# Performance work log

Hardware: AMD Instinct MI355X
Metric: run time of the kernel (lower is better)

## Reference

```python
import jax, jax.numpy as jnp
import numpy as np

HIDDEN = 1024
INTER = 2048
NUM_EXPERTS = 8
TOPK = 2
STD = 0.02


def setup_inputs() -> dict:
    key = jax.random.key(0)
    k1, k2, k3, k4 = jax.random.split(key, 4)
    return {
        "hidden_states": jax.random.normal(k1, (1, 2048, HIDDEN), dtype=jnp.float32),
        "w1": jax.random.normal(k2, (NUM_EXPERTS, 2 * INTER, HIDDEN), dtype=jnp.float32) * STD,
        "w2": jax.random.normal(k3, (NUM_EXPERTS, HIDDEN, INTER), dtype=jnp.float32) * STD,
        "router_w": jax.random.normal(k4, (NUM_EXPERTS, HIDDEN), dtype=jnp.float32) * STD,
    }


def reference(hidden_states, w1, w2, router_w):
    # renormalize=False (the torch forward's default)
    orig_shape = hidden_states.shape
    dtype = hidden_states.dtype
    x = hidden_states.reshape(-1, orig_shape[-1])          # [T, H]
    E = w1.shape[0]

    gating = x @ router_w.T                                 # [T, E]
    probs = jax.nn.softmax(gating.astype(jnp.float32), axis=-1)
    topk_w, sel = jax.lax.top_k(probs, TOPK)                # [T, K]
    topk_w = topk_w.astype(dtype)

    # Per-(token, expert) combine weight; equivalent to the dispatch/sort/
    # grouped-GEMM/index_add path since unselected experts get weight 0.
    combine = (jax.nn.one_hot(sel, E, dtype=dtype) * topk_w[..., None]).sum(axis=1)  # [T, E]

    h = jnp.einsum('td,eid->tei', x, w1)                    # [T, E, 2*INTER]
    gate = jax.nn.silu(h[..., :INTER])
    y = h[..., INTER:] * gate                               # [T, E, INTER]
    out = jnp.einsum('tei,ehi,te->th', y, w2, combine)      # [T, H]
    return out.reshape(orig_shape)
```

## Files before the change

kernel.cpp:

```cpp
#include <hip/hip_runtime.h>
#include <hip/hip_bf16.h>
#include <math.h>

#define T_TOKENS 2048
#define HID 1024
#define INTER 2048
#define NE 8

typedef __attribute__((ext_vector_type(8))) __bf16 bf16x8;
typedef __attribute__((ext_vector_type(4))) __bf16 bf16x4;
typedef __attribute__((ext_vector_type(4))) float f32x4;

#define WS_COUNTS   0u
#define WS_OFFSETS  64u
#define WS_SEL      128u
#define WS_SELW     16512u
#define WS_ROWTOK   32896u
#define WS_ROWW     49280u
#define WS_XB       131072u
#define WS_Y        (131072u + 4194304u)

__device__ __forceinline__ void gload_lds16(const void* g, void* l) {
    __builtin_amdgcn_global_load_lds(
        (const __attribute__((address_space(1))) unsigned int*)g,
        (__attribute__((address_space(3))) unsigned int*)l, 16, 0, 0);
}

__device__ __forceinline__ bf16x8 cvt8(float4 a, float4 b) {
    bf16x8 r;
    r[0] = (__bf16)a.x; r[1] = (__bf16)a.y; r[2] = (__bf16)a.z; r[3] = (__bf16)a.w;
    r[4] = (__bf16)b.x; r[5] = (__bf16)b.y; r[6] = (__bf16)b.z; r[7] = (__bf16)b.w;
    return r;
}

__device__ __forceinline__ bf16x8 ldsfrag(const __bf16* base, int row, int g) {
    return *(const bf16x8*)((const char*)base + row * 64 +
                            ((g ^ ((row >> 1) & 3)) << 4));
}

__global__ __launch_bounds__(256) void moe_router(
    const float* __restrict__ x, const float* __restrict__ rw,
    int* __restrict__ counts, int* __restrict__ sel, float* __restrict__ selw,
    __bf16* __restrict__ xb)
{
    int wave = threadIdx.x >> 6;
    int lane = threadIdx.x & 63;
    int t = blockIdx.x * 4 + wave;
    if (t >= T_TOKENS) return;

    const float4* x4  = (const float4*)x + (size_t)t * (HID / 4);
    const float4* rw4 = (const float4*)rw;

    float acc[NE];
#pragma unroll
    for (int e = 0; e < NE; ++e) acc[e] = 0.f;
#pragma unroll
    for (int q = 0; q < 4; ++q) {
        int idx = q * 64 + lane;
        float4 xv = x4[idx];
        bf16x4 c;
        c[0] = (__bf16)xv.x; c[1] = (__bf16)xv.y; c[2] = (__bf16)xv.z; c[3] = (__bf16)xv.w;
        *(bf16x4*)(xb + (size_t)t * HID + idx * 4) = c;
#pragma unroll
        for (int e = 0; e < NE; ++e) {
            float4 rv = rw4[e * (HID / 4) + idx];
            acc[e] += xv.x * rv.x + xv.y * rv.y + xv.z * rv.z + xv.w * rv.w;
        }
    }
#pragma unroll
    for (int off = 32; off; off >>= 1)
#pragma unroll
        for (int e = 0; e < NE; ++e) acc[e] += __shfl_xor(acc[e], off, 64);

    if (lane == 0) {
        float m = acc[0];
#pragma unroll
        for (int e = 1; e < NE; ++e) m = fmaxf(m, acc[e]);
        float p[NE], s = 0.f;
#pragma unroll
        for (int e = 0; e < NE; ++e) { p[e] = expf(acc[e] - m); s += p[e]; }
        float inv = 1.f / s;
        int i0 = 0;
#pragma unroll
        for (int e = 1; e < NE; ++e) if (p[e] > p[i0]) i0 = e;
        int i1 = (i0 == 0) ? 1 : 0;
#pragma unroll
        for (int e = 0; e < NE; ++e) if (e != i0 && p[e] > p[i1]) i1 = e;
        sel[t * 2 + 0] = i0; selw[t * 2 + 0] = p[i0] * inv;
        sel[t * 2 + 1] = i1; selw[t * 2 + 1] = p[i1] * inv;
        atomicAdd(&counts[i0], 1);
        atomicAdd(&counts[i1], 1);
    }
}

__global__ __launch_bounds__(256) void moe_scan_assign(
    const int* __restrict__ counts, int* __restrict__ offsets,
    const int* __restrict__ sel, const float* __restrict__ selw,
    int* __restrict__ row_token, float* __restrict__ row_w)
{
    __shared__ int soff[NE];
    __shared__ int scur[NE];
    if (threadIdx.x == 0) {
        int off = 0;
        for (int e = 0; e < NE; ++e) { soff[e] = off; off += counts[e]; }
    }
    if (threadIdx.x < NE) scur[threadIdx.x] = 0;
    __syncthreads();
    if (threadIdx.x < NE) offsets[threadIdx.x] = soff[threadIdx.x];
    for (int t = threadIdx.x; t < T_TOKENS; t += 256) {
#pragma unroll
        for (int k = 0; k < 2; ++k) {
            int e = sel[t * 2 + k];
            int slot = atomicAdd(&scur[e], 1);
            int r = soff[e] + slot;
            row_token[r] = t;
            row_w[r] = selw[t * 2 + k];
        }
    }
}

__global__ __launch_bounds__(256, 4) void moe_gemm1(
    const __bf16* __restrict__ xb, const float* __restrict__ w1,
    const int* __restrict__ row_token, const int* __restrict__ counts,
    const int* __restrict__ offsets, __bf16* __restrict__ y)
{
    int e = blockIdx.z;
    int cnt = counts[e];
    int row0 = blockIdx.y * 128;
    if (row0 >= cnt) return;
    int col0 = blockIdx.x * 64;
    int base = offsets[e];

    __shared__ __bf16 As[2][128 * 32];
    __shared__ __bf16 Bg[2][64 * 32];
    __shared__ __bf16 Bu[2][64 * 32];

    int tid = threadIdx.x;
    int lane = tid & 63;
    int wid = tid >> 6;
    int gq = tid & 3;
    int sw = (tid >> 3) & 3;

    const __bf16* srcA[2];
    int dstA[2];
#pragma unroll
    for (int i = 0; i < 2; ++i) {
        int r = i * 64 + (tid >> 2);
        int rl = row0 + r; if (rl > cnt - 1) rl = cnt - 1;
        int tok = row_token[base + rl];
        srcA[i] = xb + (size_t)tok * HID + ((gq ^ sw) << 3);
        dstA[i] = i * 4096 + tid * 16;
    }
    int rb = tid >> 2;
    const float* srcBg = w1 + ((size_t)e * 2 * INTER + col0 + rb) * HID + (gq << 3);
    const float* srcBu = srcBg + (size_t)INTER * HID;
    int offB = rb * 64 + ((gq ^ sw) << 4);

#pragma unroll
    for (int i = 0; i < 2; ++i) gload_lds16(srcA[i], (char*)As[0] + dstA[i]);
    {
        float4 g0 = *(const float4*)(srcBg);
        float4 g1 = *(const float4*)(srcBg + 4);
        float4 u0 = *(const float4*)(srcBu);
        float4 u1 = *(const float4*)(srcBu + 4);
        *(bf16x8*)((char*)Bg[0] + offB) = cvt8(g0, g1);
        *(bf16x8*)((char*)Bu[0] + offB) = cvt8(u0, u1);
    }
    __syncthreads();

    int wr = (wid >> 1) * 64, wc = (wid & 1) * 32;
    f32x4 ag[4][2] = {}, au[4][2] = {};

    for (int t = 0; t < 32; ++t) {
        int cur = t & 1;
        float4 g0, g1, u0, u1;
        bool pre = (t < 31);
        if (pre) {
            int k0 = (t + 1) * 32;
#pragma unroll
            for (int i = 0; i < 2; ++i)
                gload_lds16(srcA[i] + k0, (char*)As[cur ^ 1] + dstA[i]);
            g0 = *(const float4*)(srcBg + k0);
            g1 = *(const float4*)(srcBg + k0 + 4);
            u0 = *(const float4*)(srcBu + k0);
            u1 = *(const float4*)(srcBu + k0 + 4);
        }
        const __bf16* Ab = As[cur];
        const __bf16* Bgb = Bg[cur];
        const __bf16* Bub = Bu[cur];
        {
            int kg = lane >> 4;
            bf16x8 a[4], bg[2], bu[2];
#pragma unroll
            for (int m = 0; m < 4; ++m) a[m] = ldsfrag(Ab, wr + m * 16 + (lane & 15), kg);
#pragma unroll
            for (int n = 0; n < 2; ++n) {
                bg[n] = ldsfrag(Bgb, wc + n * 16 + (lane & 15), kg);
                bu[n] = ldsfrag(Bub, wc + n * 16 + (lane & 15), kg);
            }
#pragma unroll
            for (int m = 0; m < 4; ++m)
#pragma unroll
                for (int n = 0; n < 2; ++n) {
                    ag[m][n] = __builtin_amdgcn_mfma_f32_16x16x32_bf16(a[m], bg[n], ag[m][n], 0, 0, 0);
                    au[m][n] = __builtin_amdgcn_mfma_f32_16x16x32_bf16(a[m], bu[n], au[m][n], 0, 0, 0);
                }
        }
        if (pre) {
            *(bf16x8*)((char*)Bg[cur ^ 1] + offB) = cvt8(g0, g1);
            *(bf16x8*)((char*)Bu[cur ^ 1] + offB) = cvt8(u0, u1);
        }
        __syncthreads();
    }

#pragma unroll
    for (int m = 0; m < 4; ++m) {
#pragma unroll
        for (int j = 0; j < 4; ++j) {
            int rl = wr + m * 16 + ((lane >> 4) << 2) + j;
            if (row0 + rl >= cnt) continue;
            size_t yrow = (size_t)(base + row0 + rl) * INTER;
#pragma unroll
            for (int n = 0; n < 2; ++n) {
                float g = ag[m][n][j], u = au[m][n][j];
                float s = g / (1.f + __expf(-g));
                y[yrow + col0 + wc + n * 16 + (lane & 15)] = (__bf16)(s * u);
            }
        }
    }
}

__global__ __launch_bounds__(256, 4) void moe_gemm2(
    const __bf16* __restrict__ y, const float* __restrict__ w2,
    const float* __restrict__ row_w, const int* __restrict__ row_token,
    const int* __restrict__ counts, const int* __restrict__ offsets,
    float* __restrict__ out)
{
    int e = blockIdx.z;
    int cnt = counts[e];
    int row0 = (blockIdx.y >> 1) * 128;
    if (row0 >= cnt) return;
    int kbase = (blockIdx.y & 1) * (INTER / 2);
    int col0 = blockIdx.x * 64;
    int base = offsets[e];

    __shared__ __bf16 As[2][128 * 32];
    __shared__ __bf16 Bs[2][64 * 32];

    int tid = threadIdx.x;
    int lane = tid & 63;
    int wid = tid >> 6;
    int gq = tid & 3;
    int sw = (tid >> 3) & 3;

    const __bf16* srcA[2];
    int dstA[2];
#pragma unroll
    for (int i = 0; i < 2; ++i) {
        int r = i * 64 + (tid >> 2);
        int rl = row0 + r; if (rl > cnt - 1) rl = cnt - 1;
        srcA[i] = y + (size_t)(base + rl) * INTER + kbase + ((gq ^ sw) << 3);
        dstA[i] = i * 4096 + tid * 16;
    }
    int rb = tid >> 2;
    const float* srcB = w2 + ((size_t)e * HID + col0 + rb) * INTER + kbase + (gq << 3);
    int offB = rb * 64 + ((gq ^ sw) << 4);

#pragma unroll
    for (int i = 0; i < 2; ++i) gload_lds16(srcA[i], (char*)As[0] + dstA[i]);
    {
        float4 b0 = *(const float4*)(srcB);
        float4 b1 = *(const float4*)(srcB + 4);
        *(bf16x8*)((char*)Bs[0] + offB) = cvt8(b0, b1);
    }
    __syncthreads();

    int wr = (wid >> 1) * 64, wc = (wid & 1) * 32;
    f32x4 acc[4][2] = {};

    for (int t = 0; t < 32; ++t) {
        int cur = t & 1;
        float4 b0, b1;
        bool pre = (t < 31);
        if (pre) {
            int k0 = (t + 1) * 32;
#pragma unroll
            for (int i = 0; i < 2; ++i)
                gload_lds16(srcA[i] + k0, (char*)As[cur ^ 1] + dstA[i]);
            b0 = *(const float4*)(srcB + k0);
            b1 = *(const float4*)(srcB + k0 + 4);
        }
        const __bf16* Ab = As[cur];
        const __bf16* Bb = Bs[cur];
        {
            int kg = lane >> 4;
            bf16x8 a[4], b[2];
#pragma unroll
            for (int m = 0; m < 4; ++m) a[m] = ldsfrag(Ab, wr + m * 16 + (lane & 15), kg);
#pragma unroll
            for (int n = 0; n < 2; ++n) b[n] = ldsfrag(Bb, wc + n * 16 + (lane & 15), kg);
#pragma unroll
            for (int m = 0; m < 4; ++m)
#pragma unroll
                for (int n = 0; n < 2; ++n)
                    acc[m][n] = __builtin_amdgcn_mfma_f32_16x16x32_bf16(a[m], b[n], acc[m][n], 0, 0, 0);
        }
        if (pre) {
            *(bf16x8*)((char*)Bs[cur ^ 1] + offB) = cvt8(b0, b1);
        }
        __syncthreads();
    }

#pragma unroll
    for (int m = 0; m < 4; ++m) {
#pragma unroll
        for (int j = 0; j < 4; ++j) {
            int rl = wr + m * 16 + ((lane >> 4) << 2) + j;
            if (row0 + rl >= cnt) continue;
            float wgt = row_w[base + row0 + rl];
            int tok = row_token[base + row0 + rl];
#pragma unroll
            for (int n = 0; n < 2; ++n)
                atomicAdd(&out[(size_t)tok * HID + col0 + wc + n * 16 + (lane & 15)],
                          acc[m][n][j] * wgt);
        }
    }
}

extern "C" void kernel_launch(void* const* d_in, const int* in_sizes, int n_in,
                              void* d_out, int out_size, void* d_ws, size_t ws_size,
                              hipStream_t stream) {
    const float* x  = (const float*)d_in[0];
    const float* w1 = (const float*)d_in[1];
    const float* w2 = (const float*)d_in[2];
    const float* rw = (const float*)d_in[3];
    float* out = (float*)d_out;

    char* ws = (char*)d_ws;
    int*    counts     = (int*)(ws + WS_COUNTS);
    int*    offsets    = (int*)(ws + WS_OFFSETS);
    int*    sel        = (int*)(ws + WS_SEL);
    float*  selw       = (float*)(ws + WS_SELW);
    int*    row_token  = (int*)(ws + WS_ROWTOK);
    float*  row_w      = (float*)(ws + WS_ROWW);
    __bf16* xb         = (__bf16*)(ws + WS_XB);
    __bf16* y          = (__bf16*)(ws + WS_Y);

    hipMemsetAsync(ws, 0, 128, stream);
    hipMemsetAsync(out, 0, (size_t)T_TOKENS * HID * sizeof(float), stream);

    moe_router<<<T_TOKENS / 4, 256, 0, stream>>>(x, rw, counts, sel, selw, xb);
    moe_scan_assign<<<1, 256, 0, stream>>>(counts, offsets, sel, selw,
                                           row_token, row_w);
    moe_gemm1<<<dim3(INTER / 64, 16, NE), 256, 0, stream>>>(
        xb, w1, row_token, counts, offsets, y);
    moe_gemm2<<<dim3(HID / 64, 32, NE), 256, 0, stream>>>(
        y, w2, row_w, row_token, counts, offsets, out);
}
```

Before: 423.8 us.

## Load fp32 weights directly to LDS and convert at fragment read time

Both grouped GEMMs now stream the fp32 weight tiles straight into shared memory with global_load_lds instead of loading through registers and converting before the LDS store. The bf16 conversion moves into the fragment read, and the K step grows to 64 with an XOR swizzle on both tiles. Double buffering is dropped for a single buffer bracketed by two barriers, and occupancy hints fall from 4 to 3 blocks. GEMM2 switches to a 128-wide N tile with a 4-way K split. The goal is to cut register pressure and the VALU conversion cost, at the price of more LDS (fp32 B tiles) and no overlap between loads and MFMA work.

```diff
diff --git a/kernel.cpp b/kernel.cpp
--- a/kernel.cpp
+++ b/kernel.cpp
@@ -33,9 +33,16 @@
     return r;
 }
 
-__device__ __forceinline__ bf16x8 ldsfrag(const __bf16* base, int row, int g) {
-    return *(const bf16x8*)((const char*)base + row * 64 +
-                            ((g ^ ((row >> 1) & 3)) << 4));
+__device__ __forceinline__ bf16x8 ldsfragA(const __bf16* base, int row, int g) {
+    return *(const bf16x8*)((const char*)base + row * 128 + ((g ^ (row & 7)) << 4));
+}
+
+__device__ __forceinline__ bf16x8 ldsfragB(const float* base, int row, int kc4) {
+    const char* p = (const char*)base + row * 256;
+    int s = row & 7;
+    float4 p0 = *(const float4*)(p + ((((kc4 << 1)    ) ^ s) << 4));
+    float4 p1 = *(const float4*)(p + ((((kc4 << 1) | 1) ^ s) << 4));
+    return cvt8(p0, p1);
 }
 
 __global__ __launch_bounds__(256) void moe_router(
@@ -119,7 +126,7 @@
     }
 }
 
-__global__ __launch_bounds__(256, 4) void moe_gemm1(
+__global__ __launch_bounds__(256, 3) void moe_gemm1(
     const __bf16* __restrict__ xb, const float* __restrict__ w1,
     const int* __restrict__ row_token, const int* __restrict__ counts,
     const int* __restrict__ offsets, __bf16* __restrict__ y)
@@ -131,72 +138,60 @@
     int col0 = blockIdx.x * 64;
     int base = offsets[e];
 
-    __shared__ __bf16 As[2][128 * 32];
-    __shared__ __bf16 Bg[2][64 * 32];
-    __shared__ __bf16 Bu[2][64 * 32];
+    __shared__ __bf16 As[128 * 64];
+    __shared__ float  Bs[128 * 64];
 
     int tid = threadIdx.x;
     int lane = tid & 63;
     int wid = tid >> 6;
-    int gq = tid & 3;
-    int sw = (tid >> 3) & 3;
-
-    const __bf16* srcA[2];
-    int dstA[2];
-#pragma unroll
-    for (int i = 0; i < 2; ++i) {
-        int r = i * 64 + (tid >> 2);
+
+    const __bf16* srcA[4];
+    int dstA[4];
+#pragma unroll
+    for (int i = 0; i < 4; ++i) {
+        int ii = wid * 4 + i;
+        int r = ii * 8 + (lane >> 3);
         int rl = row0 + r; if (rl > cnt - 1) rl = cnt - 1;
         int tok = row_token[base + rl];
-        srcA[i] = xb + (size_t)tok * HID + ((gq ^ sw) << 3);
-        dstA[i] = i * 4096 + tid * 16;
-    }
-    int rb = tid >> 2;
-    const float* srcBg = w1 + ((size_t)e * 2 * INTER + col0 + rb) * HID + (gq << 3);
-    const float* srcBu = srcBg + (size_t)INTER * HID;
-    int offB = rb * 64 + ((gq ^ sw) << 4);
-
-#pragma unroll
-    for (int i = 0; i < 2; ++i) gload_lds16(srcA[i], (char*)As[0] + dstA[i]);
+        srcA[i] = xb + (size_t)tok * HID + (((lane & 7) ^ (r & 7)) << 3);
+        dstA[i] = ii * 1024 + lane * 16;
+    }
+    const float* srcB[2];
+    int dstB0 = wid * 8192 + lane * 16;
     {
-        float4 g0 = *(const float4*)(srcBg);
-        float4 g1 = *(const float4*)(srcBg + 4);
-        float4 u0 = *(const float4*)(srcBu);
-        float4 u1 = *(const float4*)(srcBu + 4);
-        *(bf16x8*)((char*)Bg[0] + offB) = cvt8(g0, g1);
-        *(bf16x8*)((char*)Bu[0] + offB) = cvt8(u0, u1);
-    }
-    __syncthreads();
+        int rev = wid * 32 + (lane >> 4);
+        int rod = rev + 4;
+        int grow_ev = (rev < 64) ? (col0 + rev) : (INTER + col0 + rev - 64);
+        int grow_od = (rod < 64) ? (col0 + rod) : (INTER + col0 + rod - 64);
+        srcB[0] = w1 + ((size_t)e * 2 * INTER + grow_ev) * HID
+                     + (((lane & 15) ^ (rev & 7)) << 2);
+        srcB[1] = w1 + ((size_t)e * 2 * INTER + grow_od) * HID
+                     + (((lane & 15) ^ (rod & 7)) << 2);
+    }
 
     int wr = (wid >> 1) * 64, wc = (wid & 1) * 32;
     f32x4 ag[4][2] = {}, au[4][2] = {};
 
-    for (int t = 0; t < 32; ++t) {
-        int cur = t & 1;
-        float4 g0, g1, u0, u1;
-        bool pre = (t < 31);
-        if (pre) {
-            int k0 = (t + 1) * 32;
-#pragma unroll
-            for (int i = 0; i < 2; ++i)
-                gload_lds16(srcA[i] + k0, (char*)As[cur ^ 1] + dstA[i]);
-            g0 = *(const float4*)(srcBg + k0);
-            g1 = *(const float4*)(srcBg + k0 + 4);
-            u0 = *(const float4*)(srcBu + k0);
-            u1 = *(const float4*)(srcBu + k0 + 4);
-        }
-        const __bf16* Ab = As[cur];
-        const __bf16* Bgb = Bg[cur];
-        const __bf16* Bub = Bu[cur];
-        {
-            int kg = lane >> 4;
+    for (int k0 = 0; k0 < HID; k0 += 64) {
+        __syncthreads();
+#pragma unroll
+        for (int i = 0; i < 4; ++i)
+            gload_lds16(srcA[i] + k0, (char*)As + dstA[i]);
+#pragma unroll
+        for (int i = 0; i < 8; ++i)
+            gload_lds16(srcB[i & 1] + (i >> 1) * (8 * HID) + k0,
+                        (char*)Bs + dstB0 + i * 1024);
+        __syncthreads();
+#pragma unroll
+        for (int ks = 0; ks < 2; ++ks) {
+            int kc4 = ks * 4 + (lane >> 4);
             bf16x8 a[4], bg[2], bu[2];
 #pragma unroll
-            for (int m = 0; m < 4; ++m) a[m] = ldsfrag(Ab, wr + m * 16 + (lane & 15), kg);
+            for (int m = 0; m < 4; ++m) a[m] = ldsfragA(As, wr + m * 16 + (lane & 15), kc4);
 #pragma unroll
             for (int n = 0; n < 2; ++n) {
-                bg[n] = ldsfrag(Bgb, wc + n * 16 + (lane & 15), kg);
-                bu[n] = ldsfrag(Bub, wc + n * 16 + (lane & 15), kg);
+                bg[n] = ldsfragB(Bs, wc + n * 16 + (lane & 15), kc4);
+                bu[n] = ldsfragB(Bs, 64 + wc + n * 16 + (lane & 15), kc4);
             }
 #pragma unroll
             for (int m = 0; m < 4; ++m)
@@ -206,11 +201,6 @@
                     au[m][n] = __builtin_amdgcn_mfma_f32_16x16x32_bf16(a[m], bu[n], au[m][n], 0, 0, 0);
                 }
         }
-        if (pre) {
-            *(bf16x8*)((char*)Bg[cur ^ 1] + offB) = cvt8(g0, g1);
-            *(bf16x8*)((char*)Bu[cur ^ 1] + offB) = cvt8(u0, u1);
-        }
-        __syncthreads();
     }
 
 #pragma unroll
@@ -230,7 +220,7 @@
     }
 }
 
-__global__ __launch_bounds__(256, 4) void moe_gemm2(
+__global__ __launch_bounds__(256, 3) void moe_gemm2(
     const __bf16* __restrict__ y, const float* __restrict__ w2,
     const float* __restrict__ row_w, const int* __restrict__ row_token,
     const int* __restrict__ counts, const int* __restrict__ offsets,
@@ -238,77 +228,67 @@
 {
     int e = blockIdx.z;
     int cnt = counts[e];
-    int row0 = (blockIdx.y >> 1) * 128;
+    int row0 = (blockIdx.y >> 2) * 128;
     if (row0 >= cnt) return;
-    int kbase = (blockIdx.y & 1) * (INTER / 2);
-    int col0 = blockIdx.x * 64;
+    int kbase = (blockIdx.y & 3) * (INTER / 4);
+    int col0 = blockIdx.x * 128;
     int base = offsets[e];
 
-    __shared__ __bf16 As[2][128 * 32];
-    __shared__ __bf16 Bs[2][64 * 32];
+    __shared__ __bf16 As[128 * 64];
+    __shared__ float  Bs[128 * 64];
 
     int tid = threadIdx.x;
     int lane = tid & 63;
     int wid = tid >> 6;
-    int gq = tid & 3;
-    int sw = (tid >> 3) & 3;
-
-    const __bf16* srcA[2];
-    int dstA[2];
-#pragma unroll
-    for (int i = 0; i < 2; ++i) {
-        int r = i * 64 + (tid >> 2);
+
+    const __bf16* srcA[4];
+    int dstA[4];
+#pragma unroll
+    for (int i = 0; i < 4; ++i) {
+        int ii = wid * 4 + i;
+        int r = ii * 8 + (lane >> 3);
         int rl = row0 + r; if (rl > cnt - 1) rl = cnt - 1;
-        srcA[i] = y + (size_t)(base + rl) * INTER + kbase + ((gq ^ sw) << 3);
-        dstA[i] = i * 4096 + tid * 16;
-    }
-    int rb = tid >> 2;
-    const float* srcB = w2 + ((size_t)e * HID + col0 + rb) * INTER + kbase + (gq << 3);
-    int offB = rb * 64 + ((gq ^ sw) << 4);
-
-#pragma unroll
-    for (int i = 0; i < 2; ++i) gload_lds16(srcA[i], (char*)As[0] + dstA[i]);
+        srcA[i] = y + (size_t)(base + rl) * INTER + kbase + (((lane & 7) ^ (r & 7)) << 3);
+        dstA[i] = ii * 1024 + lane * 16;
+    }
+    const float* srcB[2];
+    int dstB0 = wid * 8192 + lane * 16;
     {
-        float4 b0 = *(const float4*)(srcB);
-        float4 b1 = *(const float4*)(srcB + 4);
-        *(bf16x8*)((char*)Bs[0] + offB) = cvt8(b0, b1);
-    }
-    __syncthreads();
-
-    int wr = (wid >> 1) * 64, wc = (wid & 1) * 32;
-    f32x4 acc[4][2] = {};
-
-    for (int t = 0; t < 32; ++t) {
-        int cur = t & 1;
-        float4 b0, b1;
-        bool pre = (t < 31);
-        if (pre) {
-            int k0 = (t + 1) * 32;
-#pragma unroll
-            for (int i = 0; i < 2; ++i)
-                gload_lds16(srcA[i] + k0, (char*)As[cur ^ 1] + dstA[i]);
-            b0 = *(const float4*)(srcB + k0);
-            b1 = *(const float4*)(srcB + k0 + 4);
-        }
-        const __bf16* Ab = As[cur];
-        const __bf16* Bb = Bs[cur];
-        {
-            int kg = lane >> 4;
-            bf16x8 a[4], b[2];
-#pragma unroll
-            for (int m = 0; m < 4; ++m) a[m] = ldsfrag(Ab, wr + m * 16 + (lane & 15), kg);
-#pragma unroll
-            for (int n = 0; n < 2; ++n) b[n] = ldsfrag(Bb, wc + n * 16 + (lane & 15), kg);
+        int rev = wid * 32 + (lane >> 4);
+        int rod = rev + 4;
+        srcB[0] = w2 + ((size_t)e * HID + col0 + rev) * INTER + kbase
+                     + (((lane & 15) ^ (rev & 7)) << 2);
+        srcB[1] = w2 + ((size_t)e * HID + col0 + rod) * INTER + kbase
+                     + (((lane & 15) ^ (rod & 7)) << 2);
+    }
+
+    int wr = (wid >> 1) * 64, wc = (wid & 1) * 64;
+    f32x4 acc[4][4] = {};
+
+    for (int k0 = 0; k0 < INTER / 4; k0 += 64) {
+        __syncthreads();
+#pragma unroll
+        for (int i = 0; i < 4; ++i)
+            gload_lds16(srcA[i] + k0, (char*)As + dstA[i]);
+#pragma unroll
+        for (int i = 0; i < 8; ++i)
+            gload_lds16(srcB[i & 1] + (i >> 1) * (8 * INTER) + k0,
+                        (char*)Bs + dstB0 + i * 1024);
+        __syncthreads();
+#pragma unroll
+        for (int ks = 0; ks < 2; ++ks) {
+            int kc4 = ks * 4 + (lane >> 4);
+            bf16x8 a[4], b[4];
+#pragma unroll
+            for (int m = 0; m < 4; ++m) a[m] = ldsfragA(As, wr + m * 16 + (lane & 15), kc4);
+#pragma unroll
+            for (int n = 0; n < 4; ++n) b[n] = ldsfragB(Bs, wc + n * 16 + (lane & 15), kc4);
 #pragma unroll
             for (int m = 0; m < 4; ++m)
 #pragma unroll
-                for (int n = 0; n < 2; ++n)
+                for (int n = 0; n < 4; ++n)
                     acc[m][n] = __builtin_amdgcn_mfma_f32_16x16x32_bf16(a[m], b[n], acc[m][n], 0, 0, 0);
         }
-        if (pre) {
-            *(bf16x8*)((char*)Bs[cur ^ 1] + offB) = cvt8(b0, b1);
-        }
-        __syncthreads();
     }
 
 #pragma unroll
@@ -320,7 +300,7 @@
             float wgt = row_w[base + row0 + rl];
             int tok = row_token[base + row0 + rl];
 #pragma unroll
-            for (int n = 0; n < 2; ++n)
+            for (int n = 0; n < 4; ++n)
                 atomicAdd(&out[(size_t)tok * HID + col0 + wc + n * 16 + (lane & 15)],
                           acc[m][n][j] * wgt);
         }
@@ -354,6 +334,6 @@
                                            row_token, row_w);
     moe_gemm1<<<dim3(INTER / 64, 16, NE), 256, 0, stream>>>(
         xb, w1, row_token, counts, offsets, y);
-    moe_gemm2<<<dim3(HID / 64, 32, NE), 256, 0, stream>>>(
+    moe_gemm2<<<dim3(HID / 128, 64, NE), 256, 0, stream>>>(
         y, w2, row_w, row_token, counts, offsets, out);
 }
```

Result: faster. 406.1 us (-4.2%).
